# Performance work log

Hardware: AMD Instinct MI355X
Metric: run time of the kernel (lower is better)

The kernel has to match this reference:

```python
import jax, jax.numpy as jnp
import numpy as np

D_MODEL = 1024
H = 16
D_K = D_MODEL // H
NEG = -1e9


def setup_inputs() -> dict:
    key = jax.random.key(0)
    ks = jax.random.split(key, 12)
    B, S = 4, 2048
    scale = 1.0 / np.sqrt(D_MODEL)
    return {
        "q": jax.random.normal(ks[0], (B, S, D_MODEL), dtype=jnp.float32),
        "k": jax.random.normal(ks[1], (B, S, D_MODEL), dtype=jnp.float32),
        "v": jax.random.normal(ks[2], (B, S, D_MODEL), dtype=jnp.float32),
        "mask": jnp.ones((1, 1, S, S), dtype=jnp.int32),
        "w_q": jax.random.normal(ks[3], (D_MODEL, D_MODEL), dtype=jnp.float32) * scale,
        "b_q": jnp.zeros((D_MODEL,), dtype=jnp.float32),
        "w_k": jax.random.normal(ks[4], (D_MODEL, D_MODEL), dtype=jnp.float32) * scale,
        "b_k": jnp.zeros((D_MODEL,), dtype=jnp.float32),
        "w_v": jax.random.normal(ks[5], (D_MODEL, D_MODEL), dtype=jnp.float32) * scale,
        "b_v": jnp.zeros((D_MODEL,), dtype=jnp.float32),
        "w_o": jax.random.normal(ks[6], (D_MODEL, D_MODEL), dtype=jnp.float32) * scale,
        "b_o": jnp.zeros((D_MODEL,), dtype=jnp.float32),
    }


def reference(q, k, v, mask, w_q, b_q, w_k, b_k, w_v, b_v, w_o, b_o):
    B, S, _ = q.shape
    # projections (torch Linear: x @ W^T + b)
    query = q @ w_q.T + b_q
    key = k @ w_k.T + b_k
    value = v @ w_v.T + b_v
    # [B, S, D] -> [B, H, S, d_k]
    query = query.reshape(B, S, H, D_K).transpose(0, 2, 1, 3)
    key = key.reshape(B, S, H, D_K).transpose(0, 2, 1, 3)
    value = value.reshape(B, S, H, D_K).transpose(0, 2, 1, 3)
    # scaled dot-product attention, full [B,H,S,S] scores as in original
    scores = jnp.einsum("bhqd,bhkd->bhqk", query, key) / jnp.sqrt(
        jnp.asarray(D_K, dtype=query.dtype)
    )
    scores = jnp.where(mask == 0, jnp.asarray(NEG, dtype=scores.dtype), scores)
    attn = jax.nn.softmax(scores, axis=-1)
    x = jnp.einsum("bhqk,bhkd->bhqd", attn, value)
    # [B, H, S, d_k] -> [B, S, D]
    x = x.transpose(0, 2, 1, 3).reshape(B, S, H * D_K)
    return x @ w_o.T + b_o
```

## Files before the change

### kernel.cpp

```cpp
#include <hip/hip_runtime.h>

typedef unsigned short u16;
typedef unsigned int u32;
typedef unsigned long long u64;
typedef __attribute__((ext_vector_type(8))) short short8;
typedef __attribute__((ext_vector_type(4))) float f32x4;
typedef __attribute__((ext_vector_type(16))) float f32x16;
typedef __attribute__((ext_vector_type(4))) u32 u32x4;

constexpr int S_LEN = 2048;
constexpr int DMODEL = 1024;

#if __has_builtin(__builtin_amdgcn_exp2f)
#define EXP2 __builtin_amdgcn_exp2f
#else
#define EXP2 exp2f
#endif

__device__ __forceinline__ u16 f2bf(float f) {
  u32 u = __builtin_bit_cast(u32, f);
  u += 0x7FFFu + ((u >> 16) & 1u);
  return (u16)(u >> 16);
}

__device__ __forceinline__ u32 cvtpk(float a, float b) {
  u32 r;
  asm("v_cvt_pk_bf16_f32 %0, %1, %2" : "=v"(r) : "v"(a), "v"(b));
  return r;
}

__device__ __forceinline__ void plswap(u32& a, u32& b) {
  asm("v_permlane32_swap_b32 %0, %1" : "+v"(a), "+v"(b));
}

__device__ __forceinline__ void gload_lds16(const void* g, void* l) {
  __builtin_amdgcn_global_load_lds((const __attribute__((address_space(1))) u32*)g,
                                   (__attribute__((address_space(3))) u32*)l,
                                   16, 0, 0);
}

__global__ __launch_bounds__(256) void cvt_w_kernel(
    const float* __restrict__ w0, const float* __restrict__ w1,
    const float* __restrict__ w2, const float* __restrict__ w3,
    u16* __restrict__ o0, u16* __restrict__ o1,
    u16* __restrict__ o2, u16* __restrict__ o3) {
  const float* src; u16* dst;
  switch (blockIdx.y) {
    case 0: src = w0; dst = o0; break;
    case 1: src = w1; dst = o1; break;
    case 2: src = w2; dst = o2; break;
    default: src = w3; dst = o3; break;
  }
  int i = blockIdx.x * 256 + threadIdx.x;
  float4 v = ((const float4*)src)[i];
  ushort4 h;
  h.x = f2bf(v.x); h.y = f2bf(v.y); h.z = f2bf(v.z); h.w = f2bf(v.w);
  ((ushort4*)dst)[i] = h;
}

__global__ __launch_bounds__(256) void mask_pack_kernel(
    const int* __restrict__ mask, u64* __restrict__ mb) {
  int gw = (blockIdx.x * 256 + threadIdx.x) >> 6;
  int lane = threadIdx.x & 63;
  #pragma unroll
  for (int i = 0; i < 16; ++i) {
    size_t word = (size_t)gw * 16 + i;
    int m = mask[word * 64 + lane];
    u64 bits = __ballot(m != 0);
    if (lane == 0) mb[word] = bits;
  }
}

__global__ __launch_bounds__(256) void vt_kernel(
    const u16* __restrict__ Vp, u16* __restrict__ VpT) {
  __shared__ u16 T[64][72];
  const int st = blockIdx.x, bh = blockIdx.y;
  const int b = bh >> 4, h = bh & 15;
  const int s0 = st * 64;
  const int tid = threadIdx.x;
  #pragma unroll
  for (int i = 0; i < 2; ++i) {
    int g = tid + i * 256;
    int sr = g >> 3, c8 = g & 7;
    short8 v = *(const short8*)(Vp + ((size_t)(b * S_LEN + s0 + sr)) * DMODEL + h * 64 + c8 * 8);
    *(short8*)&T[sr][c8 * 8] = v;
  }
  __syncthreads();
  #pragma unroll
  for (int i = 0; i < 2; ++i) {
    int g = tid + i * 256;
    int d = g >> 3, s8 = g & 7;
    short8 o;
    #pragma unroll
    for (int j = 0; j < 8; ++j) o[j] = T[s8 * 8 + j][d];
    *(short8*)(VpT + ((size_t)(bh * 64 + d)) * S_LEN + s0 + s8 * 8) = o;
  }
}

template<bool AF32, bool OUTF32>
__global__ __launch_bounds__(256) void gemm_bt_kernel(
    const void* __restrict__ Av, const u16* __restrict__ W,
    const float* __restrict__ bias, void* __restrict__ Cv, float scale) {
  constexpr int BK = 32;
  __shared__ __align__(16) u16 As[128 * BK];
  __shared__ __align__(16) u16 Bs[128 * BK];
  const int tid = threadIdx.x;
  const int lane = tid & 63, w = tid >> 6;
  const int l15 = lane & 15, lg = lane >> 4;
  const int m0 = blockIdx.x * 128, n0 = blockIdx.y * 128;
  const int wm = w >> 1, wn = w & 1;
  f32x4 acc[4][4] = {};

  for (int kt = 0; kt < 1024; kt += BK) {
    #pragma unroll
    for (int j = 0; j < 2; ++j) {
      int sb = (w * 2 + j) * 64;
      int slot = sb + lane;
      int row = slot >> 2, c8 = slot & 3;
      gload_lds16(W + (size_t)(n0 + row) * 1024 + kt + c8 * 8,
                  (char*)Bs + (size_t)sb * 16);
    }
    if constexpr (AF32) {
      const float* A = (const float*)Av;
      #pragma unroll
      for (int i = 0; i < 4; ++i) {
        int slot = tid + i * 256;
        int row = slot >> 3, c4 = slot & 7;
        float4 v = *(const float4*)(A + (size_t)(m0 + row) * 1024 + kt + c4 * 4);
        ushort4 h;
        h.x = f2bf(v.x); h.y = f2bf(v.y); h.z = f2bf(v.z); h.w = f2bf(v.w);
        *(ushort4*)&As[row * BK + c4 * 4] = h;
      }
    } else {
      const u16* A = (const u16*)Av;
      #pragma unroll
      for (int j = 0; j < 2; ++j) {
        int sb = (w * 2 + j) * 64;
        int slot = sb + lane;
        int row = slot >> 2, c8 = slot & 3;
        gload_lds16(A + (size_t)(m0 + row) * 1024 + kt + c8 * 8,
                    (char*)As + (size_t)sb * 16);
      }
    }
    __syncthreads();
    short8 af[4], bfr[4];
    #pragma unroll
    for (int m = 0; m < 4; ++m)
      af[m] = *(const short8*)&As[(wm * 64 + m * 16 + l15) * BK + lg * 8];
    #pragma unroll
    for (int n = 0; n < 4; ++n)
      bfr[n] = *(const short8*)&Bs[(wn * 64 + n * 16 + l15) * BK + lg * 8];
    #pragma unroll
    for (int m = 0; m < 4; ++m)
      #pragma unroll
      for (int n = 0; n < 4; ++n)
        acc[m][n] = __builtin_amdgcn_mfma_f32_16x16x32_bf16(af[m], bfr[n], acc[m][n], 0, 0, 0);
    __syncthreads();
  }

  #pragma unroll
  for (int m = 0; m < 4; ++m) {
    #pragma unroll
    for (int n = 0; n < 4; ++n) {
      int col = n0 + wn * 64 + n * 16 + l15;
      float bcol = bias[col];
      #pragma unroll
      for (int r = 0; r < 4; ++r) {
        int row = m0 + wm * 64 + m * 16 + lg * 4 + r;
        float v = (acc[m][n][r] + bcol) * scale;
        if constexpr (OUTF32)
          ((float*)Cv)[(size_t)row * 1024 + col] = v;
        else
          ((u16*)Cv)[(size_t)row * 1024 + col] = f2bf(v);
      }
    }
  }
}

__global__ __launch_bounds__(256, 4) void attn_kernel(
    const u16* __restrict__ Qp, const u16* __restrict__ Kp,
    const u16* __restrict__ VpT, const u64* __restrict__ mb,
    u16* __restrict__ X) {
  constexpr float NEGL2 = -1.4426950e9f;
  __shared__ __align__(16) u16 Ks[2][4096];
  __shared__ __align__(16) u16 VTs[2][4096];
  const int tid = threadIdx.x;
  const int lane = tid & 63, w = tid >> 6;
  const int l31 = lane & 31, hi1 = lane >> 5;

  u32 id = blockIdx.x;
  u32 nid = ((id & 7) << 7) | (id >> 3);
  const int bh = nid >> 4, qt = nid & 15;
  const int b = bh >> 4, h = bh & 15;
  const size_t bS = (size_t)b * S_LEN;
  const int wq0 = qt * 128 + w * 32;

  short8 qf[4];
  {
    const u16* qb = Qp + (bS + wq0 + l31) * DMODEL + h * 64;
    #pragma unroll
    for (int dk = 0; dk < 4; ++dk)
      qf[dk] = *(const short8*)(qb + dk * 16 + hi1 * 8);
  }

  f32x16 xacc[2] = {};
  float lsum = 0.f;

  auto stage = [&](int k0, int nb) {
    #pragma unroll
    for (int i = 0; i < 2; ++i) {
      int g = tid + i * 256;
      int kk = g >> 3, dh = g & 7;
      gload_lds16(Kp + (bS + k0 + kk) * DMODEL + h * 64 + ((dh ^ (kk & 7)) << 3),
                  (char*)&Ks[nb][0] + g * 16);
    }
    #pragma unroll
    for (int i = 0; i < 2; ++i) {
      int g = tid + i * 256;
      int dd = g >> 3, kh = g & 7;
      gload_lds16(VpT + ((size_t)(bh * 64 + dd)) * S_LEN + k0 + ((kh ^ (dd & 7)) << 3),
                  (char*)&VTs[nb][0] + g * 16);
    }
  };

  stage(0, 0);
  __syncthreads();

  constexpr int NT = S_LEN / 64;
  for (int t = 0; t < NT; ++t) {
    const int cur = t & 1;
    if (t + 1 < NT) stage((t + 1) * 64, cur ^ 1);

    f32x16 c0, c1;
    #pragma unroll
    for (int r = 0; r < 16; ++r) { c0[r] = -16.f; c1[r] = -16.f; }
    const u16* ksp = &Ks[cur][0];
    __builtin_amdgcn_s_setprio(1);
    #pragma unroll
    for (int dk = 0; dk < 4; ++dk) {
      short8 a0 = *(const short8*)&ksp[((l31) * 64 + dk * 16 + hi1 * 8) ^ ((l31 & 7) << 3)];
      short8 a1 = *(const short8*)&ksp[((32 + l31) * 64 + dk * 16 + hi1 * 8) ^ ((l31 & 7) << 3)];
      c0 = __builtin_amdgcn_mfma_f32_32x32x16_bf16(a0, qf[dk], c0, 0, 0, 0);
      c1 = __builtin_amdgcn_mfma_f32_32x32x16_bf16(a1, qf[dk], c1, 0, 0, 0);
    }
    __builtin_amdgcn_s_setprio(0);

    u64 mw = mb[(size_t)(wq0 + l31) * 32 + t];
    bool allone = __all((long long)mw == -1LL);
    if (!allone) {
      #pragma unroll
      for (int r = 0; r < 16; ++r) {
        int k0i = (r & 3) + 8 * (r >> 2) + 4 * hi1;
        c0[r] = ((mw >> k0i) & 1) ? c0[r] : NEGL2;
        c1[r] = ((mw >> (k0i + 32)) & 1) ? c1[r] : NEGL2;
      }
    }

    float ls = 0.f;
    #pragma unroll
    for (int r = 0; r < 16; ++r) { float p = EXP2(c0[r]); c0[r] = p; ls += p; }
    #pragma unroll
    for (int r = 0; r < 16; ++r) { float p = EXP2(c1[r]); c1[r] = p; ls += p; }
    lsum += ls;

    u32 Wp[2][8];
    #pragma unroll
    for (int i = 0; i < 8; ++i) {
      Wp[0][i] = cvtpk(c0[2 * i], c0[2 * i + 1]);
      Wp[1][i] = cvtpk(c1[2 * i], c1[2 * i + 1]);
    }

    const u16* vtp = &VTs[cur][0];
    __builtin_amdgcn_s_setprio(1);
    #pragma unroll
    for (int ks16 = 0; ks16 < 4; ++ks16) {
      const int kc = ks16 >> 1, ks = ks16 & 1;
      u32 wa0 = Wp[kc][ks * 4 + 0], wb0 = Wp[kc][ks * 4 + 2];
      u32 wa1 = Wp[kc][ks * 4 + 1], wb1 = Wp[kc][ks * 4 + 3];
      plswap(wa0, wb0);
      plswap(wa1, wb1);
      u32x4 pw; pw.x = wa0; pw.y = wa1; pw.z = wb0; pw.w = wb1;
      short8 pfrag = __builtin_bit_cast(short8, pw);
      #pragma unroll
      for (int dt = 0; dt < 2; ++dt) {
        int d = dt * 32 + l31;
        short8 vf = *(const short8*)&vtp[(d * 64 + ks16 * 16 + hi1 * 8) ^ ((d & 7) << 3)];
        xacc[dt] = __builtin_amdgcn_mfma_f32_32x32x16_bf16(vf, pfrag, xacc[dt], 0, 0, 0);
      }
    }
    __builtin_amdgcn_s_setprio(0);
    __syncthreads();
  }

  lsum += __shfl_xor(lsum, 32);
  float inv = 1.0f / lsum;
  u16* xb = X + (bS + wq0 + l31) * DMODEL + h * 64;
  #pragma unroll
  for (int dt = 0; dt < 2; ++dt)
    #pragma unroll
    for (int m = 0; m < 4; ++m) {
      ushort4 o;
      o.x = f2bf(xacc[dt][m * 4 + 0] * inv);
      o.y = f2bf(xacc[dt][m * 4 + 1] * inv);
      o.z = f2bf(xacc[dt][m * 4 + 2] * inv);
      o.w = f2bf(xacc[dt][m * 4 + 3] * inv);
      *(ushort4*)(xb + dt * 32 + m * 8 + hi1 * 4) = o;
    }
}

extern "C" void kernel_launch(void* const* d_in, const int* in_sizes, int n_in,
                              void* d_out, int out_size, void* d_ws, size_t ws_size,
                              hipStream_t stream) {
  const float* q  = (const float*)d_in[0];
  const float* k  = (const float*)d_in[1];
  const float* v  = (const float*)d_in[2];
  const int* mask = (const int*)d_in[3];
  const float* wq = (const float*)d_in[4];
  const float* bq = (const float*)d_in[5];
  const float* wk = (const float*)d_in[6];
  const float* bk = (const float*)d_in[7];
  const float* wv = (const float*)d_in[8];
  const float* bv = (const float*)d_in[9];
  const float* wo = (const float*)d_in[10];
  const float* bo = (const float*)d_in[11];

  char* ws = (char*)d_ws;
  u16* wqb = (u16*)(ws + 0x000000);
  u16* wkb = (u16*)(ws + 0x200000);
  u16* wvb = (u16*)(ws + 0x400000);
  u16* wob = (u16*)(ws + 0x600000);
  u64* mbp = (u64*)(ws + 0x800000);
  u16* Qp  = (u16*)(ws + 0x880000);
  u16* Kp  = (u16*)(ws + 0x1880000);
  u16* Vp  = (u16*)(ws + 0x2880000);
  u16* Xp  = (u16*)(ws + 0x3880000);
  u16* VpT = (u16*)(ws + 0x4880000);

  const float QSCALE = 0.125f * 1.44269504088896340736f;

  cvt_w_kernel<<<dim3(1024, 4), 256, 0, stream>>>(wq, wk, wv, wo, wqb, wkb, wvb, wob);
  mask_pack_kernel<<<1024, 256, 0, stream>>>(mask, mbp);
  gemm_bt_kernel<true, false><<<dim3(64, 8), 256, 0, stream>>>(q, wqb, bq, Qp, QSCALE);
  gemm_bt_kernel<true, false><<<dim3(64, 8), 256, 0, stream>>>(k, wkb, bk, Kp, 1.0f);
  gemm_bt_kernel<true, false><<<dim3(64, 8), 256, 0, stream>>>(v, wvb, bv, Vp, 1.0f);
  vt_kernel<<<dim3(32, 64), 256, 0, stream>>>(Vp, VpT);
  attn_kernel<<<1024, 256, 0, stream>>>(Qp, Kp, VpT, mbp, Xp);
  gemm_bt_kernel<false, true><<<dim3(64, 8), 256, 0, stream>>>(Xp, wob, bo, (float*)d_out, 1.0f);
}
```

Baseline: 283.7 us.

## Double query rows per attention wave and pre-convert activations to bf16

Each attention wave now handles two 32-row query tiles, reusing the K and V fragments it loads from LDS for both tiles. This halves the number of attention blocks and lowers the occupancy hint from 4 to 2. The projection GEMMs no longer convert fp32 activations inline: a separate conversion kernel writes a bf16 copy into the X buffer, and the GEMM then loads both operands directly into LDS. The trade-off is extra launches and extra global traffic for the converted copies, plus higher register pressure in the attention kernel.

```diff
diff --git a/kernel.cpp b/kernel.cpp
--- a/kernel.cpp
+++ b/kernel.cpp
@@ -51,6 +51,15 @@
     case 2: src = w2; dst = o2; break;
     default: src = w3; dst = o3; break;
   }
+  int i = blockIdx.x * 256 + threadIdx.x;
+  float4 v = ((const float4*)src)[i];
+  ushort4 h;
+  h.x = f2bf(v.x); h.y = f2bf(v.y); h.z = f2bf(v.z); h.w = f2bf(v.w);
+  ((ushort4*)dst)[i] = h;
+}
+
+__global__ __launch_bounds__(256) void cvt_a_kernel(
+    const float* __restrict__ src, u16* __restrict__ dst) {
   int i = blockIdx.x * 256 + threadIdx.x;
   float4 v = ((const float4*)src)[i];
   ushort4 h;
@@ -97,9 +106,9 @@
   }
 }
 
-template<bool AF32, bool OUTF32>
+template<bool OUTF32>
 __global__ __launch_bounds__(256) void gemm_bt_kernel(
-    const void* __restrict__ Av, const u16* __restrict__ W,
+    const u16* __restrict__ A, const u16* __restrict__ W,
     const float* __restrict__ bias, void* __restrict__ Cv, float scale) {
   constexpr int BK = 32;
   __shared__ __align__(16) u16 As[128 * BK];
@@ -119,28 +128,8 @@
       int row = slot >> 2, c8 = slot & 3;
       gload_lds16(W + (size_t)(n0 + row) * 1024 + kt + c8 * 8,
                   (char*)Bs + (size_t)sb * 16);
-    }
-    if constexpr (AF32) {
-      const float* A = (const float*)Av;
-      #pragma unroll
-      for (int i = 0; i < 4; ++i) {
-        int slot = tid + i * 256;
-        int row = slot >> 3, c4 = slot & 7;
-        float4 v = *(const float4*)(A + (size_t)(m0 + row) * 1024 + kt + c4 * 4);
-        ushort4 h;
-        h.x = f2bf(v.x); h.y = f2bf(v.y); h.z = f2bf(v.z); h.w = f2bf(v.w);
-        *(ushort4*)&As[row * BK + c4 * 4] = h;
-      }
-    } else {
-      const u16* A = (const u16*)Av;
-      #pragma unroll
-      for (int j = 0; j < 2; ++j) {
-        int sb = (w * 2 + j) * 64;
-        int slot = sb + lane;
-        int row = slot >> 2, c8 = slot & 3;
-        gload_lds16(A + (size_t)(m0 + row) * 1024 + kt + c8 * 8,
-                    (char*)As + (size_t)sb * 16);
-      }
+      gload_lds16(A + (size_t)(m0 + row) * 1024 + kt + c8 * 8,
+                  (char*)As + (size_t)sb * 16);
     }
     __syncthreads();
     short8 af[4], bfr[4];
@@ -177,7 +166,7 @@
   }
 }
 
-__global__ __launch_bounds__(256, 4) void attn_kernel(
+__global__ __launch_bounds__(256, 2) void attn_kernel(
     const u16* __restrict__ Qp, const u16* __restrict__ Kp,
     const u16* __restrict__ VpT, const u64* __restrict__ mb,
     u16* __restrict__ X) {
@@ -189,22 +178,25 @@
   const int l31 = lane & 31, hi1 = lane >> 5;
 
   u32 id = blockIdx.x;
-  u32 nid = ((id & 7) << 7) | (id >> 3);
-  const int bh = nid >> 4, qt = nid & 15;
+  u32 nid = ((id & 7) << 6) | (id >> 3);
+  const int bh = nid >> 3, qt = nid & 7;
   const int b = bh >> 4, h = bh & 15;
   const size_t bS = (size_t)b * S_LEN;
-  const int wq0 = qt * 128 + w * 32;
-
-  short8 qf[4];
+  const int wq0 = qt * 256 + w * 64;
+
+  short8 qfA[4], qfB[4];
   {
-    const u16* qb = Qp + (bS + wq0 + l31) * DMODEL + h * 64;
-    #pragma unroll
-    for (int dk = 0; dk < 4; ++dk)
-      qf[dk] = *(const short8*)(qb + dk * 16 + hi1 * 8);
-  }
-
-  f32x16 xacc[2] = {};
-  float lsum = 0.f;
+    const u16* qa = Qp + (bS + wq0 + l31) * DMODEL + h * 64;
+    const u16* qb = Qp + (bS + wq0 + 32 + l31) * DMODEL + h * 64;
+    #pragma unroll
+    for (int dk = 0; dk < 4; ++dk) {
+      qfA[dk] = *(const short8*)(qa + dk * 16 + hi1 * 8);
+      qfB[dk] = *(const short8*)(qb + dk * 16 + hi1 * 8);
+    }
+  }
+
+  f32x16 xaccA[2] = {}, xaccB[2] = {};
+  float lsA = 0.f, lsB = 0.f;
 
   auto stage = [&](int k0, int nb) {
     #pragma unroll
@@ -231,43 +223,82 @@
     const int cur = t & 1;
     if (t + 1 < NT) stage((t + 1) * 64, cur ^ 1);
 
-    f32x16 c0, c1;
-    #pragma unroll
-    for (int r = 0; r < 16; ++r) { c0[r] = -16.f; c1[r] = -16.f; }
     const u16* ksp = &Ks[cur][0];
-    __builtin_amdgcn_s_setprio(1);
+    short8 a0[4], a1[4];
     #pragma unroll
     for (int dk = 0; dk < 4; ++dk) {
-      short8 a0 = *(const short8*)&ksp[((l31) * 64 + dk * 16 + hi1 * 8) ^ ((l31 & 7) << 3)];
-      short8 a1 = *(const short8*)&ksp[((32 + l31) * 64 + dk * 16 + hi1 * 8) ^ ((l31 & 7) << 3)];
-      c0 = __builtin_amdgcn_mfma_f32_32x32x16_bf16(a0, qf[dk], c0, 0, 0, 0);
-      c1 = __builtin_amdgcn_mfma_f32_32x32x16_bf16(a1, qf[dk], c1, 0, 0, 0);
-    }
-    __builtin_amdgcn_s_setprio(0);
-
-    u64 mw = mb[(size_t)(wq0 + l31) * 32 + t];
-    bool allone = __all((long long)mw == -1LL);
-    if (!allone) {
-      #pragma unroll
-      for (int r = 0; r < 16; ++r) {
-        int k0i = (r & 3) + 8 * (r >> 2) + 4 * hi1;
-        c0[r] = ((mw >> k0i) & 1) ? c0[r] : NEGL2;
-        c1[r] = ((mw >> (k0i + 32)) & 1) ? c1[r] : NEGL2;
-      }
-    }
-
-    float ls = 0.f;
-    #pragma unroll
-    for (int r = 0; r < 16; ++r) { float p = EXP2(c0[r]); c0[r] = p; ls += p; }
-    #pragma unroll
-    for (int r = 0; r < 16; ++r) { float p = EXP2(c1[r]); c1[r] = p; ls += p; }
-    lsum += ls;
-
-    u32 Wp[2][8];
-    #pragma unroll
-    for (int i = 0; i < 8; ++i) {
-      Wp[0][i] = cvtpk(c0[2 * i], c0[2 * i + 1]);
-      Wp[1][i] = cvtpk(c1[2 * i], c1[2 * i + 1]);
+      a0[dk] = *(const short8*)&ksp[((l31) * 64 + dk * 16 + hi1 * 8) ^ ((l31 & 7) << 3)];
+      a1[dk] = *(const short8*)&ksp[((32 + l31) * 64 + dk * 16 + hi1 * 8) ^ ((l31 & 7) << 3)];
+    }
+
+    u64 mwA = mb[(size_t)(wq0 + l31) * 32 + t];
+    u64 mwB = mb[(size_t)(wq0 + 32 + l31) * 32 + t];
+    bool anymask = !__all((mwA & mwB) == ~0ull);
+
+    u32 WpA[2][8], WpB[2][8];
+
+    {
+      f32x16 c0, c1;
+      #pragma unroll
+      for (int r = 0; r < 16; ++r) { c0[r] = -16.f; c1[r] = -16.f; }
+      __builtin_amdgcn_s_setprio(1);
+      #pragma unroll
+      for (int dk = 0; dk < 4; ++dk) {
+        c0 = __builtin_amdgcn_mfma_f32_32x32x16_bf16(a0[dk], qfA[dk], c0, 0, 0, 0);
+        c1 = __builtin_amdgcn_mfma_f32_32x32x16_bf16(a1[dk], qfA[dk], c1, 0, 0, 0);
+      }
+      __builtin_amdgcn_s_setprio(0);
+      if (anymask) {
+        #pragma unroll
+        for (int r = 0; r < 16; ++r) {
+          int k0i = (r & 3) + 8 * (r >> 2) + 4 * hi1;
+          c0[r] = ((mwA >> k0i) & 1) ? c0[r] : NEGL2;
+          c1[r] = ((mwA >> (k0i + 32)) & 1) ? c1[r] : NEGL2;
+        }
+      }
+      float ls = 0.f;
+      #pragma unroll
+      for (int r = 0; r < 16; ++r) { float p = EXP2(c0[r]); c0[r] = p; ls += p; }
+      #pragma unroll
+      for (int r = 0; r < 16; ++r) { float p = EXP2(c1[r]); c1[r] = p; ls += p; }
+      lsA += ls;
+      #pragma unroll
+      for (int i = 0; i < 8; ++i) {
+        WpA[0][i] = cvtpk(c0[2 * i], c0[2 * i + 1]);
+        WpA[1][i] = cvtpk(c1[2 * i], c1[2 * i + 1]);
+      }
+    }
+
+    {
+      f32x16 c0, c1;
+      #pragma unroll
+      for (int r = 0; r < 16; ++r) { c0[r] = -16.f; c1[r] = -16.f; }
+      __builtin_amdgcn_s_setprio(1);
+      #pragma unroll
+      for (int dk = 0; dk < 4; ++dk) {
+        c0 = __builtin_amdgcn_mfma_f32_32x32x16_bf16(a0[dk], qfB[dk], c0, 0, 0, 0);
+        c1 = __builtin_amdgcn_mfma_f32_32x32x16_bf16(a1[dk], qfB[dk], c1, 0, 0, 0);
+      }
+      __builtin_amdgcn_s_setprio(0);
+      if (anymask) {
+        #pragma unroll
+        for (int r = 0; r < 16; ++r) {
+          int k0i = (r & 3) + 8 * (r >> 2) + 4 * hi1;
+          c0[r] = ((mwB >> k0i) & 1) ? c0[r] : NEGL2;
+          c1[r] = ((mwB >> (k0i + 32)) & 1) ? c1[r] : NEGL2;
+        }
+      }
+      float ls = 0.f;
+      #pragma unroll
+      for (int r = 0; r < 16; ++r) { float p = EXP2(c0[r]); c0[r] = p; ls += p; }
+      #pragma unroll
+      for (int r = 0; r < 16; ++r) { float p = EXP2(c1[r]); c1[r] = p; ls += p; }
+      lsB += ls;
+      #pragma unroll
+      for (int i = 0; i < 8; ++i) {
+        WpB[0][i] = cvtpk(c0[2 * i], c0[2 * i + 1]);
+        WpB[1][i] = cvtpk(c1[2 * i], c1[2 * i + 1]);
+      }
     }
 
     const u16* vtp = &VTs[cur][0];
@@ -275,36 +306,57 @@
     #pragma unroll
     for (int ks16 = 0; ks16 < 4; ++ks16) {
       const int kc = ks16 >> 1, ks = ks16 & 1;
-      u32 wa0 = Wp[kc][ks * 4 + 0], wb0 = Wp[kc][ks * 4 + 2];
-      u32 wa1 = Wp[kc][ks * 4 + 1], wb1 = Wp[kc][ks * 4 + 3];
-      plswap(wa0, wb0);
-      plswap(wa1, wb1);
-      u32x4 pw; pw.x = wa0; pw.y = wa1; pw.z = wb0; pw.w = wb1;
-      short8 pfrag = __builtin_bit_cast(short8, pw);
+      short8 vf[2];
       #pragma unroll
       for (int dt = 0; dt < 2; ++dt) {
         int d = dt * 32 + l31;
-        short8 vf = *(const short8*)&vtp[(d * 64 + ks16 * 16 + hi1 * 8) ^ ((d & 7) << 3)];
-        xacc[dt] = __builtin_amdgcn_mfma_f32_32x32x16_bf16(vf, pfrag, xacc[dt], 0, 0, 0);
+        vf[dt] = *(const short8*)&vtp[(d * 64 + ks16 * 16 + hi1 * 8) ^ ((d & 7) << 3)];
+      }
+      {
+        u32 wa0 = WpA[kc][ks * 4 + 0], wb0 = WpA[kc][ks * 4 + 2];
+        u32 wa1 = WpA[kc][ks * 4 + 1], wb1 = WpA[kc][ks * 4 + 3];
+        plswap(wa0, wb0);
+        plswap(wa1, wb1);
+        u32x4 pw; pw.x = wa0; pw.y = wa1; pw.z = wb0; pw.w = wb1;
+        short8 pfrag = __builtin_bit_cast(short8, pw);
+        xaccA[0] = __builtin_amdgcn_mfma_f32_32x32x16_bf16(vf[0], pfrag, xaccA[0], 0, 0, 0);
+        xaccA[1] = __builtin_amdgcn_mfma_f32_32x32x16_bf16(vf[1], pfrag, xaccA[1], 0, 0, 0);
+      }
+      {
+        u32 wa0 = WpB[kc][ks * 4 + 0], wb0 = WpB[kc][ks * 4 + 2];
+        u32 wa1 = WpB[kc][ks * 4 + 1], wb1 = WpB[kc][ks * 4 + 3];
+        plswap(wa0, wb0);
+        plswap(wa1, wb1);
+        u32x4 pw; pw.x = wa0; pw.y = wa1; pw.z = wb0; pw.w = wb1;
+        short8 pfrag = __builtin_bit_cast(short8, pw);
+        xaccB[0] = __builtin_amdgcn_mfma_f32_32x32x16_bf16(vf[0], pfrag, xaccB[0], 0, 0, 0);
+        xaccB[1] = __builtin_amdgcn_mfma_f32_32x32x16_bf16(vf[1], pfrag, xaccB[1], 0, 0, 0);
       }
     }
     __builtin_amdgcn_s_setprio(0);
     __syncthreads();
   }
 
-  lsum += __shfl_xor(lsum, 32);
-  float inv = 1.0f / lsum;
-  u16* xb = X + (bS + wq0 + l31) * DMODEL + h * 64;
+  lsA += __shfl_xor(lsA, 32);
+  lsB += __shfl_xor(lsB, 32);
+  float invA = 1.0f / lsA, invB = 1.0f / lsB;
+  u16* xa = X + (bS + wq0 + l31) * DMODEL + h * 64;
+  u16* xb = X + (bS + wq0 + 32 + l31) * DMODEL + h * 64;
   #pragma unroll
   for (int dt = 0; dt < 2; ++dt)
     #pragma unroll
     for (int m = 0; m < 4; ++m) {
-      ushort4 o;
-      o.x = f2bf(xacc[dt][m * 4 + 0] * inv);
-      o.y = f2bf(xacc[dt][m * 4 + 1] * inv);
-      o.z = f2bf(xacc[dt][m * 4 + 2] * inv);
-      o.w = f2bf(xacc[dt][m * 4 + 3] * inv);
-      *(ushort4*)(xb + dt * 32 + m * 8 + hi1 * 4) = o;
+      ushort4 oA, oB;
+      oA.x = f2bf(xaccA[dt][m * 4 + 0] * invA);
+      oA.y = f2bf(xaccA[dt][m * 4 + 1] * invA);
+      oA.z = f2bf(xaccA[dt][m * 4 + 2] * invA);
+      oA.w = f2bf(xaccA[dt][m * 4 + 3] * invA);
+      oB.x = f2bf(xaccB[dt][m * 4 + 0] * invB);
+      oB.y = f2bf(xaccB[dt][m * 4 + 1] * invB);
+      oB.z = f2bf(xaccB[dt][m * 4 + 2] * invB);
+      oB.w = f2bf(xaccB[dt][m * 4 + 3] * invB);
+      *(ushort4*)(xa + dt * 32 + m * 8 + hi1 * 4) = oA;
+      *(ushort4*)(xb + dt * 32 + m * 8 + hi1 * 4) = oB;
     }
 }
 
@@ -337,13 +389,21 @@
   u16* VpT = (u16*)(ws + 0x4880000);
 
   const float QSCALE = 0.125f * 1.44269504088896340736f;
+  u16* Ab = Xp;
 
   cvt_w_kernel<<<dim3(1024, 4), 256, 0, stream>>>(wq, wk, wv, wo, wqb, wkb, wvb, wob);
   mask_pack_kernel<<<1024, 256, 0, stream>>>(mask, mbp);
-  gemm_bt_kernel<true, false><<<dim3(64, 8), 256, 0, stream>>>(q, wqb, bq, Qp, QSCALE);
-  gemm_bt_kernel<true, false><<<dim3(64, 8), 256, 0, stream>>>(k, wkb, bk, Kp, 1.0f);
-  gemm_bt_kernel<true, false><<<dim3(64, 8), 256, 0, stream>>>(v, wvb, bv, Vp, 1.0f);
+
+  cvt_a_kernel<<<8192, 256, 0, stream>>>(v, Ab);
+  gemm_bt_kernel<false><<<dim3(64, 8), 256, 0, stream>>>(Ab, wvb, bv, Vp, 1.0f);
   vt_kernel<<<dim3(32, 64), 256, 0, stream>>>(Vp, VpT);
-  attn_kernel<<<1024, 256, 0, stream>>>(Qp, Kp, VpT, mbp, Xp);
-  gemm_bt_kernel<false, true><<<dim3(64, 8), 256, 0, stream>>>(Xp, wob, bo, (float*)d_out, 1.0f);
-}
+
+  cvt_a_kernel<<<8192, 256, 0, stream>>>(k, Ab);
+  gemm_bt_kernel<false><<<dim3(64, 8), 256, 0, stream>>>(Ab, wkb, bk, Kp, 1.0f);
+
+  cvt_a_kernel<<<8192, 256, 0, stream>>>(q, Ab);
+  gemm_bt_kernel<false><<<dim3(64, 8), 256, 0, stream>>>(Ab, wqb, bq, Qp, QSCALE);
+
+  attn_kernel<<<512, 256, 0, stream>>>(Qp, Kp, VpT, mbp, Xp);
+  gemm_bt_kernel<true><<<dim3(64, 8), 256, 0, stream>>>(Xp, wob, bo, (float*)d_out, 1.0f);
+}
```

Result: faster. 272.5 us (-4.0%).

## Pre-convert activations to bf16 and write V projection transposed directly

Applied to the files above, without the earlier changes.

Adds a standalone fp32->bf16 conversion kernel for q/k/v, so each projection GEMM can load A tiles asynchronously into LDS instead of doing per-thread fp32 loads and conversions in the k-loop. The V projection epilogue now writes its output directly in the per-head transposed layout, which removes the separate transpose kernel and the intermediate Vp buffer. The cost is three extra conversion passes that each read 32MB and write 16MB, plus scattered 8-byte stores in the transposed epilogue.

```diff
diff --git a/kernel.cpp b/kernel.cpp
--- a/kernel.cpp
+++ b/kernel.cpp
@@ -58,6 +58,15 @@
   ((ushort4*)dst)[i] = h;
 }
 
+__global__ __launch_bounds__(256) void cvt_a_kernel(
+    const float* __restrict__ src, u16* __restrict__ dst) {
+  int i = blockIdx.x * 256 + threadIdx.x;
+  float4 v = ((const float4*)src)[i];
+  ushort4 h;
+  h.x = f2bf(v.x); h.y = f2bf(v.y); h.z = f2bf(v.z); h.w = f2bf(v.w);
+  ((ushort4*)dst)[i] = h;
+}
+
 __global__ __launch_bounds__(256) void mask_pack_kernel(
     const int* __restrict__ mask, u64* __restrict__ mb) {
   int gw = (blockIdx.x * 256 + threadIdx.x) >> 6;
@@ -71,35 +80,9 @@
   }
 }
 
-__global__ __launch_bounds__(256) void vt_kernel(
-    const u16* __restrict__ Vp, u16* __restrict__ VpT) {
-  __shared__ u16 T[64][72];
-  const int st = blockIdx.x, bh = blockIdx.y;
-  const int b = bh >> 4, h = bh & 15;
-  const int s0 = st * 64;
-  const int tid = threadIdx.x;
-  #pragma unroll
-  for (int i = 0; i < 2; ++i) {
-    int g = tid + i * 256;
-    int sr = g >> 3, c8 = g & 7;
-    short8 v = *(const short8*)(Vp + ((size_t)(b * S_LEN + s0 + sr)) * DMODEL + h * 64 + c8 * 8);
-    *(short8*)&T[sr][c8 * 8] = v;
-  }
-  __syncthreads();
-  #pragma unroll
-  for (int i = 0; i < 2; ++i) {
-    int g = tid + i * 256;
-    int d = g >> 3, s8 = g & 7;
-    short8 o;
-    #pragma unroll
-    for (int j = 0; j < 8; ++j) o[j] = T[s8 * 8 + j][d];
-    *(short8*)(VpT + ((size_t)(bh * 64 + d)) * S_LEN + s0 + s8 * 8) = o;
-  }
-}
-
-template<bool AF32, bool OUTF32>
+template<int OM>
 __global__ __launch_bounds__(256) void gemm_bt_kernel(
-    const void* __restrict__ Av, const u16* __restrict__ W,
+    const u16* __restrict__ A, const u16* __restrict__ W,
     const float* __restrict__ bias, void* __restrict__ Cv, float scale) {
   constexpr int BK = 32;
   __shared__ __align__(16) u16 As[128 * BK];
@@ -119,28 +102,8 @@
       int row = slot >> 2, c8 = slot & 3;
       gload_lds16(W + (size_t)(n0 + row) * 1024 + kt + c8 * 8,
                   (char*)Bs + (size_t)sb * 16);
-    }
-    if constexpr (AF32) {
-      const float* A = (const float*)Av;
-      #pragma unroll
-      for (int i = 0; i < 4; ++i) {
-        int slot = tid + i * 256;
-        int row = slot >> 3, c4 = slot & 7;
-        float4 v = *(const float4*)(A + (size_t)(m0 + row) * 1024 + kt + c4 * 4);
-        ushort4 h;
-        h.x = f2bf(v.x); h.y = f2bf(v.y); h.z = f2bf(v.z); h.w = f2bf(v.w);
-        *(ushort4*)&As[row * BK + c4 * 4] = h;
-      }
-    } else {
-      const u16* A = (const u16*)Av;
-      #pragma unroll
-      for (int j = 0; j < 2; ++j) {
-        int sb = (w * 2 + j) * 64;
-        int slot = sb + lane;
-        int row = slot >> 2, c8 = slot & 3;
-        gload_lds16(A + (size_t)(m0 + row) * 1024 + kt + c8 * 8,
-                    (char*)As + (size_t)sb * 16);
-      }
+      gload_lds16(A + (size_t)(m0 + row) * 1024 + kt + c8 * 8,
+                  (char*)As + (size_t)sb * 16);
     }
     __syncthreads();
     short8 af[4], bfr[4];
@@ -164,14 +127,25 @@
     for (int n = 0; n < 4; ++n) {
       int col = n0 + wn * 64 + n * 16 + l15;
       float bcol = bias[col];
-      #pragma unroll
-      for (int r = 0; r < 4; ++r) {
-        int row = m0 + wm * 64 + m * 16 + lg * 4 + r;
-        float v = (acc[m][n][r] + bcol) * scale;
-        if constexpr (OUTF32)
-          ((float*)Cv)[(size_t)row * 1024 + col] = v;
-        else
-          ((u16*)Cv)[(size_t)row * 1024 + col] = f2bf(v);
+      int row0 = m0 + wm * 64 + m * 16 + lg * 4;
+      if constexpr (OM == 2) {
+        int b = row0 >> 11, s = row0 & 2047;
+        ushort4 o;
+        o.x = f2bf((acc[m][n][0] + bcol) * scale);
+        o.y = f2bf((acc[m][n][1] + bcol) * scale);
+        o.z = f2bf((acc[m][n][2] + bcol) * scale);
+        o.w = f2bf((acc[m][n][3] + bcol) * scale);
+        u16* dst = (u16*)Cv + ((size_t)(b * 16 + (col >> 6)) * 64 + (col & 63)) * S_LEN + s;
+        *(ushort4*)dst = o;
+      } else {
+        #pragma unroll
+        for (int r = 0; r < 4; ++r) {
+          float v = (acc[m][n][r] + bcol) * scale;
+          if constexpr (OM == 1)
+            ((float*)Cv)[(size_t)(row0 + r) * 1024 + col] = v;
+          else
+            ((u16*)Cv)[(size_t)(row0 + r) * 1024 + col] = f2bf(v);
+        }
       }
     }
   }
@@ -332,18 +306,24 @@
   u64* mbp = (u64*)(ws + 0x800000);
   u16* Qp  = (u16*)(ws + 0x880000);
   u16* Kp  = (u16*)(ws + 0x1880000);
-  u16* Vp  = (u16*)(ws + 0x2880000);
   u16* Xp  = (u16*)(ws + 0x3880000);
   u16* VpT = (u16*)(ws + 0x4880000);
 
   const float QSCALE = 0.125f * 1.44269504088896340736f;
+  u16* Ab = Xp;
 
   cvt_w_kernel<<<dim3(1024, 4), 256, 0, stream>>>(wq, wk, wv, wo, wqb, wkb, wvb, wob);
   mask_pack_kernel<<<1024, 256, 0, stream>>>(mask, mbp);
-  gemm_bt_kernel<true, false><<<dim3(64, 8), 256, 0, stream>>>(q, wqb, bq, Qp, QSCALE);
-  gemm_bt_kernel<true, false><<<dim3(64, 8), 256, 0, stream>>>(k, wkb, bk, Kp, 1.0f);
-  gemm_bt_kernel<true, false><<<dim3(64, 8), 256, 0, stream>>>(v, wvb, bv, Vp, 1.0f);
-  vt_kernel<<<dim3(32, 64), 256, 0, stream>>>(Vp, VpT);
+
+  cvt_a_kernel<<<8192, 256, 0, stream>>>(v, Ab);
+  gemm_bt_kernel<2><<<dim3(64, 8), 256, 0, stream>>>(Ab, wvb, bv, VpT, 1.0f);
+
+  cvt_a_kernel<<<8192, 256, 0, stream>>>(k, Ab);
+  gemm_bt_kernel<0><<<dim3(64, 8), 256, 0, stream>>>(Ab, wkb, bk, Kp, 1.0f);
+
+  cvt_a_kernel<<<8192, 256, 0, stream>>>(q, Ab);
+  gemm_bt_kernel<0><<<dim3(64, 8), 256, 0, stream>>>(Ab, wqb, bq, Qp, QSCALE);
+
   attn_kernel<<<1024, 256, 0, stream>>>(Qp, Kp, VpT, mbp, Xp);
-  gemm_bt_kernel<false, true><<<dim3(64, 8), 256, 0, stream>>>(Xp, wob, bo, (float*)d_out, 1.0f);
-}
+  gemm_bt_kernel<1><<<dim3(64, 8), 256, 0, stream>>>(Xp, wob, bo, (float*)d_out, 1.0f);
+}
```

Measured after the change: 245.1 us. 13.6% less time.
